# Performance work log

Measured on AMD Instinct MI355X. Metric: run time of the kernel, lower is better.

Reference implementation:

```python
import jax, jax.numpy as jnp
import numpy as np

N, L, D = 2048, 200, 64
NUM_USERS, NUM_ITEMS, NUM_R = 100000, 100000, 5


def _lin(x, W, b):
    # torch nn.Linear convention: W is [out, in]
    return x @ W.T + b


def setup_inputs() -> dict:
    key = jax.random.key(0)
    ks = jax.random.split(key, 12)
    s = 0.05
    return dict(
        nodes=jax.random.randint(ks[0], (N,), 0, NUM_ITEMS),
        history_uv=jax.random.randint(ks[1], (N, L), 0, NUM_USERS),
        history_r=jax.random.randint(ks[2], (N, L), 0, NUM_R),
        u2e=jax.random.normal(ks[3], (NUM_USERS, D), dtype=jnp.float32) * s,
        v2e=jax.random.normal(ks[4], (NUM_ITEMS, D), dtype=jnp.float32) * s,
        r2e=jax.random.normal(ks[5], (NUM_R, D), dtype=jnp.float32) * s,
        w_r1_w=jax.random.normal(ks[6], (D, 2 * D), dtype=jnp.float32) * s,
        w_r1_b=jnp.zeros((D,), jnp.float32),
        w_r2_w=jax.random.normal(ks[7], (D, D), dtype=jnp.float32) * s,
        w_r2_b=jnp.zeros((D,), jnp.float32),
        mu_w=jax.random.normal(ks[8], (D, 2 * D), dtype=jnp.float32) * s,
        mu_b=jnp.zeros((D,), jnp.float32),
        att1_w=jax.random.normal(ks[9], (D, 2 * D), dtype=jnp.float32) * s,
        att1_b=jnp.zeros((D,), jnp.float32),
        att2_w=jax.random.normal(ks[10], (D, D), dtype=jnp.float32) * s,
        att2_b=jnp.zeros((D,), jnp.float32),
        att3_w=jax.random.normal(ks[11], (1, D), dtype=jnp.float32) * s,
        att3_b=jnp.zeros((1,), jnp.float32),
    )


def reference(nodes, history_uv, history_r, u2e, v2e, r2e,
              w_r1_w, w_r1_b, w_r2_w, w_r2_b, mu_w, mu_b,
              att1_w, att1_b, att2_w, att2_b, att3_w, att3_b):
    # uv=False branch: neighbors are users, center nodes are items
    e_uv = u2e[history_uv]                     # [N, L, D]
    q = v2e[nodes]                             # [N, D]
    e_r = r2e[history_r]                       # [N, L, D]

    x = jax.nn.relu(_lin(jnp.concatenate([e_uv, e_r], -1), w_r1_w, w_r1_b))
    o = jax.nn.relu(_lin(x, w_r2_w, w_r2_b))   # [N, L, D]

    qb = jnp.broadcast_to(q[:, None, :], o.shape)   # [N, L, D]
    g = jax.nn.sigmoid(_lin(jnp.concatenate([o, qb], -1), mu_w, mu_b))
    o = g * o + (1.0 - g) * qb                 # gated history rep

    # Attention (dropout disabled / eval mode), softmax over the L neighbors
    a = jax.nn.relu(_lin(jnp.concatenate([o, qb], -1), att1_w, att1_b))
    a = jax.nn.relu(_lin(a, att2_w, att2_b))
    a = _lin(a, att3_w, att3_b)                # [N, L, 1]
    w = jax.nn.softmax(a, axis=1)

    return jnp.sum(w * o, axis=1)              # [N, D]
```

## Files before the change

### kernel.cpp

```cpp
#include <hip/hip_runtime.h>
#include <hip/hip_bf16.h>

typedef float f32x4 __attribute__((ext_vector_type(4)));
typedef __bf16 bf16x8 __attribute__((ext_vector_type(8)));

union Frag { unsigned short h[8]; unsigned int u[4]; uint4 u4; bf16x8 b; };

__device__ __forceinline__ unsigned short f2bs(float f){
  __hip_bfloat16 v = __float2bfloat16(f);
  return __builtin_bit_cast(unsigned short, v);
}
__device__ __forceinline__ unsigned int pk2(float a, float b){
  unsigned int r;
  asm("v_cvt_pk_bf16_f32 %0, %1, %2" : "=v"(r) : "v"(a), "v"(b));
  return r;
}
__device__ __forceinline__ Frag packF(f32x4 a, f32x4 b){
  Frag f;
  f.u[0] = pk2(a[0], a[1]); f.u[1] = pk2(a[2], a[3]);
  f.u[2] = pk2(b[0], b[1]); f.u[3] = pk2(b[2], b[3]);
  return f;
}
__device__ __forceinline__ f32x4 relu4(f32x4 v){
  f32x4 r;
  #pragma unroll
  for (int j = 0; j < 4; ++j) r[j] = fmaxf(v[j], 0.f);
  return r;
}
__device__ __forceinline__ float sigmoid_fast(float x){
  return __builtin_amdgcn_rcpf(1.f + __expf(-x));
}

__global__ void prep_weights(const float* __restrict__ w1, const float* __restrict__ w2,
                             const float* __restrict__ mu, const float* __restrict__ a1,
                             const float* __restrict__ a2, const float* __restrict__ r2e,
                             uint4* __restrict__ ws){
  const int f = blockIdx.x;
  const int l = threadIdx.x;
  Frag fr;
  if (f < 64){
    const float* W; int m, s, K;
    if (f < 16)      { W = w1; m = f >> 2;        s = f & 3;        K = 128; }
    else if (f < 24) { W = w2; m = (f - 16) >> 1; s = (f - 16) & 1; K = 64;  }
    else if (f < 40) { W = mu; m = (f - 24) >> 2; s = (f - 24) & 3; K = 128; }
    else if (f < 56) { W = a1; m = (f - 40) >> 2; s = (f - 40) & 3; K = 128; }
    else             { W = a2; m = (f - 56) >> 1; s = (f - 56) & 1; K = 64;  }
    const int row = 16 * m + (l & 15);
    const int k0  = 32 * s + 4 * (l >> 4);
    #pragma unroll
    for (int h = 0; h < 2; ++h)
      #pragma unroll
      for (int j = 0; j < 4; ++j)
        fr.h[4*h + j] = f2bs(W[row * K + k0 + 16*h + j]);
    ws[f * 64 + l] = fr.u4;
  } else {
    const int f2 = f - 64;
    const int R = f2 >> 1, sp = f2 & 1;
    const int g = (l >> 4) & 3;
    #pragma unroll
    for (int h = 0; h < 2; ++h)
      #pragma unroll
      for (int j = 0; j < 4; ++j)
        fr.h[4*h + j] = f2bs(r2e[R * 64 + sp * 32 + 16*h + 4*g + j]);
    ws[4096 + f2 * 64 + l] = fr.u4;
  }
}

__global__ __launch_bounds__(256)
void uv_agg_main(const int* __restrict__ nodes, const int* __restrict__ huv,
                 const int* __restrict__ hr, const float* __restrict__ u2e,
                 const float* __restrict__ v2e,
                 const float* __restrict__ b1g, const float* __restrict__ b2g,
                 const float* __restrict__ bmg, const float* __restrict__ ba1g,
                 const float* __restrict__ ba2g, const float* __restrict__ a3g,
                 const uint4* __restrict__ wsfrag, float* __restrict__ out){
  extern __shared__ unsigned char smem[];
  uint4* wlds = (uint4*)smem;
  float* bias = (float*)(smem + 65536);
  uint4* rlds = (uint4*)(smem + 67072);

  const int tid  = threadIdx.x;
  const int lane = tid & 63;
  const int wave = tid >> 6;
  const int g    = lane >> 4;
  const int r16  = lane & 15;
  const int n    = blockIdx.x * 4 + wave;

  #pragma unroll 4
  for (int i = tid; i < 4096; i += 256) wlds[i] = wsfrag[i];
  for (int i = tid; i < 640; i += 256)  rlds[i] = wsfrag[4096 + i];
  for (int i = tid; i < 384; i += 256){
    const int w = i >> 6, d = i & 63;
    const float* src = (w==0)?b1g:(w==1)?b2g:(w==2)?bmg:(w==3)?ba1g:(w==4)?ba2g:a3g;
    bias[i] = src[d];
  }
  __syncthreads();

  const uint4* wl = wlds + lane;
  const f32x4* bl = (const f32x4*)bias + g;
  const unsigned char* rbase = (const unsigned char*)rlds + lane * 16;
  const int* hu  = huv + n * 200;
  const int* hrw = hr  + n * 200;

  const int item = nodes[n];
  f32x4 qv[4];
  #pragma unroll
  for (int m = 0; m < 4; ++m)
    qv[m] = *(const f32x4*)(v2e + (size_t)item * 64 + 16*m + 4*g);
  Frag qf[2];
  qf[0] = packF(qv[0], qv[1]); qf[1] = packF(qv[2], qv[3]);

  float swl = 0.f;
  f32x4 accw[4];
  #pragma unroll
  for (int m = 0; m < 4; ++m) accw[m] = (f32x4)(0.f);

  int irA, irB;
  f32x4 urA[4], urB[4];
  {
    const int iuA = hu[r16];      irA = hrw[r16];
    const int iuB = hu[16 + r16]; irB = hrw[16 + r16];
    const f32x4* ua = (const f32x4*)(u2e + (size_t)iuA * 64);
    const f32x4* ub = (const f32x4*)(u2e + (size_t)iuB * 64);
    #pragma unroll
    for (int s = 0; s < 4; ++s){ urA[s] = ua[4*s + g]; urB[s] = ub[4*s + g]; }
  }

  for (int it = 0; it < 7; ++it){
    Frag b0A[2], b0B[2];
    b0A[0] = packF(urA[0], urA[1]); b0A[1] = packF(urA[2], urA[3]);
    b0B[0] = packF(urB[0], urB[1]); b0B[1] = packF(urB[2], urB[3]);
    const int ircA = irA, ircB = irB;
    const bool vA = (it < 6) || (r16 < 8);
    const bool vB = (it < 6);

    if (it < 6){
      const int base = 32*it + 32;
      const int kA = min(base + r16, 199);
      const int kB = min(base + 16 + r16, 199);
      const int iuA = hu[kA]; irA = hrw[kA];
      const int iuB = hu[kB]; irB = hrw[kB];
      const f32x4* ua = (const f32x4*)(u2e + (size_t)iuA * 64);
      const f32x4* ub = (const f32x4*)(u2e + (size_t)iuB * 64);
      #pragma unroll
      for (int s = 0; s < 4; ++s){ urA[s] = ua[4*s + g]; urB[s] = ub[4*s + g]; }
    }

    f32x4 XA[4], XB[4];
    __builtin_amdgcn_s_setprio(1);
    #pragma unroll
    for (int m = 0; m < 4; ++m){
      const f32x4 bi = bl[0*16 + 4*m];
      f32x4 aA = bi, aB = bi;
      #pragma unroll
      for (int s = 0; s < 4; ++s){
        Frag w; w.u4 = wl[(m*4 + s) * 64];
        Frag eA, eB;
        if (s < 2){ eA = b0A[s]; eB = b0B[s]; }
        else {
          eA.u4 = *(const uint4*)(rbase + (size_t)(ircA*2 + (s-2)) * 1024);
          eB.u4 = *(const uint4*)(rbase + (size_t)(ircB*2 + (s-2)) * 1024);
        }
        aA = __builtin_amdgcn_mfma_f32_16x16x32_bf16(w.b, eA.b, aA, 0, 0, 0);
        aB = __builtin_amdgcn_mfma_f32_16x16x32_bf16(w.b, eB.b, aB, 0, 0, 0);
      }
      XA[m] = relu4(aA); XB[m] = relu4(aB);
    }
    __builtin_amdgcn_s_setprio(0);
    Frag bxA[2], bxB[2];
    bxA[0] = packF(XA[0], XA[1]); bxA[1] = packF(XA[2], XA[3]);
    bxB[0] = packF(XB[0], XB[1]); bxB[1] = packF(XB[2], XB[3]);

    f32x4 OA[4], OB[4];
    __builtin_amdgcn_s_setprio(1);
    #pragma unroll
    for (int m = 0; m < 4; ++m){
      const f32x4 bi = bl[1*16 + 4*m];
      f32x4 aA = bi, aB = bi;
      #pragma unroll
      for (int s = 0; s < 2; ++s){
        Frag w; w.u4 = wl[(16 + m*2 + s) * 64];
        aA = __builtin_amdgcn_mfma_f32_16x16x32_bf16(w.b, bxA[s].b, aA, 0, 0, 0);
        aB = __builtin_amdgcn_mfma_f32_16x16x32_bf16(w.b, bxB[s].b, aB, 0, 0, 0);
      }
      OA[m] = relu4(aA); OB[m] = relu4(aB);
    }
    __builtin_amdgcn_s_setprio(0);
    Frag boA[2], boB[2];
    boA[0] = packF(OA[0], OA[1]); boA[1] = packF(OA[2], OA[3]);
    boB[0] = packF(OB[0], OB[1]); boB[1] = packF(OB[2], OB[3]);

    f32x4 OGA[4], OGB[4];
    __builtin_amdgcn_s_setprio(1);
    #pragma unroll
    for (int m = 0; m < 4; ++m){
      const f32x4 bi = bl[2*16 + 4*m];
      f32x4 aA = bi, aB = bi;
      #pragma unroll
      for (int s = 0; s < 4; ++s){
        Frag w; w.u4 = wl[(24 + m*4 + s) * 64];
        const bf16x8 eA = (s < 2) ? boA[s].b : qf[s-2].b;
        const bf16x8 eB = (s < 2) ? boB[s].b : qf[s-2].b;
        aA = __builtin_amdgcn_mfma_f32_16x16x32_bf16(w.b, eA, aA, 0, 0, 0);
        aB = __builtin_amdgcn_mfma_f32_16x16x32_bf16(w.b, eB, aB, 0, 0, 0);
      }
      #pragma unroll
      for (int j = 0; j < 4; ++j){
        const float gA = sigmoid_fast(aA[j]);
        const float gB = sigmoid_fast(aB[j]);
        OGA[m][j] = fmaf(gA, OA[m][j] - qv[m][j], qv[m][j]);
        OGB[m][j] = fmaf(gB, OB[m][j] - qv[m][j], qv[m][j]);
      }
    }
    __builtin_amdgcn_s_setprio(0);
    Frag bgA[2], bgB[2];
    bgA[0] = packF(OGA[0], OGA[1]); bgA[1] = packF(OGA[2], OGA[3]);
    bgB[0] = packF(OGB[0], OGB[1]); bgB[1] = packF(OGB[2], OGB[3]);

    f32x4 A1A[4], A1B[4];
    __builtin_amdgcn_s_setprio(1);
    #pragma unroll
    for (int m = 0; m < 4; ++m){
      const f32x4 bi = bl[3*16 + 4*m];
      f32x4 aA = bi, aB = bi;
      #pragma unroll
      for (int s = 0; s < 4; ++s){
        Frag w; w.u4 = wl[(40 + m*4 + s) * 64];
        const bf16x8 eA = (s < 2) ? bgA[s].b : qf[s-2].b;
        const bf16x8 eB = (s < 2) ? bgB[s].b : qf[s-2].b;
        aA = __builtin_amdgcn_mfma_f32_16x16x32_bf16(w.b, eA, aA, 0, 0, 0);
        aB = __builtin_amdgcn_mfma_f32_16x16x32_bf16(w.b, eB, aB, 0, 0, 0);
      }
      A1A[m] = relu4(aA); A1B[m] = relu4(aB);
    }
    __builtin_amdgcn_s_setprio(0);
    Frag b4A[2], b4B[2];
    b4A[0] = packF(A1A[0], A1A[1]); b4A[1] = packF(A1A[2], A1A[3]);
    b4B[0] = packF(A1B[0], A1B[1]); b4B[1] = packF(A1B[2], A1B[3]);

    float pA = 0.f, pB = 0.f;
    __builtin_amdgcn_s_setprio(1);
    #pragma unroll
    for (int m = 0; m < 4; ++m){
      const f32x4 bi = bl[4*16 + 4*m];
      f32x4 aA = bi, aB = bi;
      #pragma unroll
      for (int s = 0; s < 2; ++s){
        Frag w; w.u4 = wl[(56 + m*2 + s) * 64];
        aA = __builtin_amdgcn_mfma_f32_16x16x32_bf16(w.b, b4A[s].b, aA, 0, 0, 0);
        aB = __builtin_amdgcn_mfma_f32_16x16x32_bf16(w.b, b4B[s].b, aB, 0, 0, 0);
      }
      aA = relu4(aA); aB = relu4(aB);
      const f32x4 a3m = bl[5*16 + 4*m];
      #pragma unroll
      for (int j = 0; j < 4; ++j){
        pA = fmaf(a3m[j], aA[j], pA);
        pB = fmaf(a3m[j], aB[j], pB);
      }
    }
    __builtin_amdgcn_s_setprio(0);
    pA += __shfl_xor(pA, 16); pA += __shfl_xor(pA, 32);
    pB += __shfl_xor(pB, 16); pB += __shfl_xor(pB, 32);

    const float eA = vA ? __expf(fminf(pA, 60.f)) : 0.f;
    const float eB = vB ? __expf(fminf(pB, 60.f)) : 0.f;
    swl += eA + eB;
    #pragma unroll
    for (int m = 0; m < 4; ++m)
      #pragma unroll
      for (int j = 0; j < 4; ++j)
        accw[m][j] = fmaf(eA, OGA[m][j], fmaf(eB, OGB[m][j], accw[m][j]));
  }

  #pragma unroll
  for (int o = 1; o < 16; o <<= 1){
    #pragma unroll
    for (int m = 0; m < 4; ++m)
      #pragma unroll
      for (int j = 0; j < 4; ++j)
        accw[m][j] += __shfl_xor(accw[m][j], o);
    swl += __shfl_xor(swl, o);
  }
  if (r16 == 0){
    const float inv = 1.f / swl;
    #pragma unroll
    for (int m = 0; m < 4; ++m){
      f32x4 v = accw[m];
      #pragma unroll
      for (int j = 0; j < 4; ++j) v[j] *= inv;
      *(f32x4*)(out + (size_t)n * 64 + 16*m + 4*g) = v;
    }
  }
}

extern "C" void kernel_launch(void* const* d_in, const int* in_sizes, int n_in,
                              void* d_out, int out_size, void* d_ws, size_t ws_size,
                              hipStream_t stream){
  const int*   nodes = (const int*)  d_in[0];
  const int*   huv   = (const int*)  d_in[1];
  const int*   hr    = (const int*)  d_in[2];
  const float* u2e   = (const float*)d_in[3];
  const float* v2e   = (const float*)d_in[4];
  const float* r2e   = (const float*)d_in[5];
  const float* w1    = (const float*)d_in[6];
  const float* b1    = (const float*)d_in[7];
  const float* w2    = (const float*)d_in[8];
  const float* b2    = (const float*)d_in[9];
  const float* muw   = (const float*)d_in[10];
  const float* mub   = (const float*)d_in[11];
  const float* a1w   = (const float*)d_in[12];
  const float* a1b   = (const float*)d_in[13];
  const float* a2w   = (const float*)d_in[14];
  const float* a2b   = (const float*)d_in[15];
  const float* a3w   = (const float*)d_in[16];

  const int N = in_sizes[0];
  uint4* ws = (uint4*)d_ws;

  hipLaunchKernelGGL(prep_weights, dim3(74), dim3(64), 0, stream,
                     w1, w2, muw, a1w, a2w, r2e, ws);
  hipLaunchKernelGGL(uv_agg_main, dim3(N / 4), dim3(256), 77312, stream,
                     nodes, huv, hr, u2e, v2e,
                     b1, b2, mub, a1b, a2b, a3w,
                     (const uint4*)ws, (float*)d_out);
}
```

Baseline: 53.24 us.

## Precompute rating and query contributions to layer pre-activations, halving K per neighbor

The rating-embedding half of the first layer is precomputed per rating value (5 rows, bias folded in) in the prep kernel and looked up from LDS, so the per-neighbor first-layer GEMM runs over K=64 instead of 128. The query halves of the gate and attention-1 layers are computed once per node before the loop and used as accumulator initialisers. This removes half of the MFMAs in three of the five per-neighbor layers and shrinks LDS. In exchange the rating contribution is now accumulated in fp32 rather than bf16, which changes numerics slightly, and the prep kernel gains a serial 64x64 dot-product block.

```diff
diff --git a/kernel.cpp b/kernel.cpp
--- a/kernel.cpp
+++ b/kernel.cpp
@@ -34,7 +34,7 @@
 __global__ void prep_weights(const float* __restrict__ w1, const float* __restrict__ w2,
                              const float* __restrict__ mu, const float* __restrict__ a1,
                              const float* __restrict__ a2, const float* __restrict__ r2e,
-                             uint4* __restrict__ ws){
+                             const float* __restrict__ b1, uint4* __restrict__ ws){
   const int f = blockIdx.x;
   const int l = threadIdx.x;
   Frag fr;
@@ -53,7 +53,7 @@
       for (int j = 0; j < 4; ++j)
         fr.h[4*h + j] = f2bs(W[row * K + k0 + 16*h + j]);
     ws[f * 64 + l] = fr.u4;
-  } else {
+  } else if (f < 74){
     const int f2 = f - 64;
     const int R = f2 >> 1, sp = f2 & 1;
     const int g = (l >> 4) & 3;
@@ -63,6 +63,15 @@
       for (int j = 0; j < 4; ++j)
         fr.h[4*h + j] = f2bs(r2e[R * 64 + sp * 32 + 16*h + 4*g + j]);
     ws[4096 + f2 * 64 + l] = fr.u4;
+  } else {
+    float* r1c = (float*)(ws + 4736);
+    const int d = l;
+    for (int R = 0; R < 5; ++R){
+      float s = b1[d];
+      for (int k = 0; k < 64; ++k)
+        s = fmaf(w1[d * 128 + 64 + k], r2e[R * 64 + k], s);
+      r1c[R * 68 + d] = s;
+    }
   }
 }
 
@@ -77,7 +86,7 @@
   extern __shared__ unsigned char smem[];
   uint4* wlds = (uint4*)smem;
   float* bias = (float*)(smem + 65536);
-  uint4* rlds = (uint4*)(smem + 67072);
+  float* r1cl = (float*)(smem + 67072);
 
   const int tid  = threadIdx.x;
   const int lane = tid & 63;
@@ -88,17 +97,19 @@
 
   #pragma unroll 4
   for (int i = tid; i < 4096; i += 256) wlds[i] = wsfrag[i];
-  for (int i = tid; i < 640; i += 256)  rlds[i] = wsfrag[4096 + i];
   for (int i = tid; i < 384; i += 256){
     const int w = i >> 6, d = i & 63;
     const float* src = (w==0)?b1g:(w==1)?b2g:(w==2)?bmg:(w==3)?ba1g:(w==4)?ba2g:a3g;
     bias[i] = src[d];
   }
+  {
+    const float* r1g = (const float*)(wsfrag + 4736);
+    for (int i = tid; i < 340; i += 256) r1cl[i] = r1g[i];
+  }
   __syncthreads();
 
   const uint4* wl = wlds + lane;
   const f32x4* bl = (const f32x4*)bias + g;
-  const unsigned char* rbase = (const unsigned char*)rlds + lane * 16;
   const int* hu  = huv + n * 200;
   const int* hrw = hr  + n * 200;
 
@@ -109,6 +120,27 @@
     qv[m] = *(const f32x4*)(v2e + (size_t)item * 64 + 16*m + 4*g);
   Frag qf[2];
   qf[0] = packF(qv[0], qv[1]); qf[1] = packF(qv[2], qv[3]);
+
+  f32x4 muq[4], a1q[4];
+  #pragma unroll
+  for (int m = 0; m < 4; ++m){
+    f32x4 a = bl[2*16 + 4*m];
+    {
+      Frag w; w.u4 = wl[(24 + m*4 + 2) * 64];
+      a = __builtin_amdgcn_mfma_f32_16x16x32_bf16(w.b, qf[0].b, a, 0, 0, 0);
+      w.u4 = wl[(24 + m*4 + 3) * 64];
+      a = __builtin_amdgcn_mfma_f32_16x16x32_bf16(w.b, qf[1].b, a, 0, 0, 0);
+    }
+    muq[m] = a;
+    f32x4 b = bl[3*16 + 4*m];
+    {
+      Frag w; w.u4 = wl[(40 + m*4 + 2) * 64];
+      b = __builtin_amdgcn_mfma_f32_16x16x32_bf16(w.b, qf[0].b, b, 0, 0, 0);
+      w.u4 = wl[(40 + m*4 + 3) * 64];
+      b = __builtin_amdgcn_mfma_f32_16x16x32_bf16(w.b, qf[1].b, b, 0, 0, 0);
+    }
+    a1q[m] = b;
+  }
 
   float swl = 0.f;
   f32x4 accw[4];
@@ -150,19 +182,13 @@
     __builtin_amdgcn_s_setprio(1);
     #pragma unroll
     for (int m = 0; m < 4; ++m){
-      const f32x4 bi = bl[0*16 + 4*m];
-      f32x4 aA = bi, aB = bi;
-      #pragma unroll
-      for (int s = 0; s < 4; ++s){
+      f32x4 aA = *(const f32x4*)&r1cl[ircA*68 + 16*m + 4*g];
+      f32x4 aB = *(const f32x4*)&r1cl[ircB*68 + 16*m + 4*g];
+      #pragma unroll
+      for (int s = 0; s < 2; ++s){
         Frag w; w.u4 = wl[(m*4 + s) * 64];
-        Frag eA, eB;
-        if (s < 2){ eA = b0A[s]; eB = b0B[s]; }
-        else {
-          eA.u4 = *(const uint4*)(rbase + (size_t)(ircA*2 + (s-2)) * 1024);
-          eB.u4 = *(const uint4*)(rbase + (size_t)(ircB*2 + (s-2)) * 1024);
-        }
-        aA = __builtin_amdgcn_mfma_f32_16x16x32_bf16(w.b, eA.b, aA, 0, 0, 0);
-        aB = __builtin_amdgcn_mfma_f32_16x16x32_bf16(w.b, eB.b, aB, 0, 0, 0);
+        aA = __builtin_amdgcn_mfma_f32_16x16x32_bf16(w.b, b0A[s].b, aA, 0, 0, 0);
+        aB = __builtin_amdgcn_mfma_f32_16x16x32_bf16(w.b, b0B[s].b, aB, 0, 0, 0);
       }
       XA[m] = relu4(aA); XB[m] = relu4(aB);
     }
@@ -194,15 +220,12 @@
     __builtin_amdgcn_s_setprio(1);
     #pragma unroll
     for (int m = 0; m < 4; ++m){
-      const f32x4 bi = bl[2*16 + 4*m];
-      f32x4 aA = bi, aB = bi;
-      #pragma unroll
-      for (int s = 0; s < 4; ++s){
+      f32x4 aA = muq[m], aB = muq[m];
+      #pragma unroll
+      for (int s = 0; s < 2; ++s){
         Frag w; w.u4 = wl[(24 + m*4 + s) * 64];
-        const bf16x8 eA = (s < 2) ? boA[s].b : qf[s-2].b;
-        const bf16x8 eB = (s < 2) ? boB[s].b : qf[s-2].b;
-        aA = __builtin_amdgcn_mfma_f32_16x16x32_bf16(w.b, eA, aA, 0, 0, 0);
-        aB = __builtin_amdgcn_mfma_f32_16x16x32_bf16(w.b, eB, aB, 0, 0, 0);
+        aA = __builtin_amdgcn_mfma_f32_16x16x32_bf16(w.b, boA[s].b, aA, 0, 0, 0);
+        aB = __builtin_amdgcn_mfma_f32_16x16x32_bf16(w.b, boB[s].b, aB, 0, 0, 0);
       }
       #pragma unroll
       for (int j = 0; j < 4; ++j){
@@ -221,15 +244,12 @@
     __builtin_amdgcn_s_setprio(1);
     #pragma unroll
     for (int m = 0; m < 4; ++m){
-      const f32x4 bi = bl[3*16 + 4*m];
-      f32x4 aA = bi, aB = bi;
-      #pragma unroll
-      for (int s = 0; s < 4; ++s){
+      f32x4 aA = a1q[m], aB = a1q[m];
+      #pragma unroll
+      for (int s = 0; s < 2; ++s){
         Frag w; w.u4 = wl[(40 + m*4 + s) * 64];
-        const bf16x8 eA = (s < 2) ? bgA[s].b : qf[s-2].b;
-        const bf16x8 eB = (s < 2) ? bgB[s].b : qf[s-2].b;
-        aA = __builtin_amdgcn_mfma_f32_16x16x32_bf16(w.b, eA, aA, 0, 0, 0);
-        aB = __builtin_amdgcn_mfma_f32_16x16x32_bf16(w.b, eB, aB, 0, 0, 0);
+        aA = __builtin_amdgcn_mfma_f32_16x16x32_bf16(w.b, bgA[s].b, aA, 0, 0, 0);
+        aB = __builtin_amdgcn_mfma_f32_16x16x32_bf16(w.b, bgB[s].b, aB, 0, 0, 0);
       }
       A1A[m] = relu4(aA); A1B[m] = relu4(aB);
     }
@@ -317,9 +337,9 @@
   const int N = in_sizes[0];
   uint4* ws = (uint4*)d_ws;
 
-  hipLaunchKernelGGL(prep_weights, dim3(74), dim3(64), 0, stream,
-                     w1, w2, muw, a1w, a2w, r2e, ws);
-  hipLaunchKernelGGL(uv_agg_main, dim3(N / 4), dim3(256), 77312, stream,
+  hipLaunchKernelGGL(prep_weights, dim3(75), dim3(64), 0, stream,
+                     w1, w2, muw, a1w, a2w, r2e, b1, ws);
+  hipLaunchKernelGGL(uv_agg_main, dim3(N / 4), dim3(256), 68432, stream,
                      nodes, huv, hr, u2e, v2e,
                      b1, b2, mub, a1b, a2b, a3w,
                      (const uint4*)ws, (float*)d_out);
```

Measured after the change: 48.10 us, median of 2. -9.7%, faster.
